# Optimization experiments

Measured on AMD Instinct MI355X. Metric: run time of the kernel, lower is better.

## Reference

```python
import jax, jax.numpy as jnp
import numpy as np

B, C, H, W = 2, 128, 96, 96
HEADS, DHEAD, WIN = 4, 32, 5
INNER = HEADS * DHEAD
PAD = WIN // 2


def setup_inputs() -> dict:
    key = jax.random.key(0)
    k1, k2, k3, k4, k5 = jax.random.split(key, 5)
    s = 1.0 / np.sqrt(C)
    return {
        "x": jax.random.normal(k1, (B, C, H, W), dtype=jnp.float32),
        "wq": jax.random.normal(k2, (INNER, C), dtype=jnp.float32) * s,
        "wk": jax.random.normal(k3, (INNER, C), dtype=jnp.float32) * s,
        "wv": jax.random.normal(k4, (INNER, C), dtype=jnp.float32) * s,
        "wproj": jax.random.normal(k5, (C, INNER), dtype=jnp.float32) * s,
    }


def _windows(t):
    # same neighborhood ordering as F.unfold (row-major over kernel offsets).
    tp = jnp.pad(t, ((0, 0), (0, 0), (0, 0), (PAD, PAD), (PAD, PAD)))
    wins = [tp[:, :, :, di:di + H, dj:dj + W]
            for di in range(WIN) for dj in range(WIN)]
    return jnp.stack(wins, axis=3)


def reference(x, wq, wk, wv, wproj):
    # 1x1 convs == per-pixel linear maps
    q = jnp.einsum('oc,bcxy->boxy', wq, x).reshape(B, HEADS, DHEAD, H, W)
    k = jnp.einsum('oc,bcxy->boxy', wk, x).reshape(B, HEADS, DHEAD, H, W)
    v = jnp.einsum('oc,bcxy->boxy', wv, x).reshape(B, HEADS, DHEAD, H, W)

    k_win = _windows(k)  # (B,h,d,25,H,W)
    v_win = _windows(v)

    scale = 1.0 / np.sqrt(DHEAD)
    attn = jnp.einsum('bhdxy,bhdkxy->bhkxy', q, k_win) * scale
    attn = jax.nn.softmax(attn, axis=2)  # softmax over the 25 window positions
    out = jnp.einsum('bhkxy,bhdkxy->bhdxy', attn, v_win)

    out = out.reshape(B, INNER, H, W)
    return jnp.einsum('co,boxy->bcxy', wproj, out)
```

## Files before the change

### kernel.cpp

```cpp
#include <hip/hip_runtime.h>
#include <hip/hip_bf16.h>
#include <hip/hip_fp16.h>

#define PP 9216
#define OO 384

typedef _Float16 f16x8 __attribute__((ext_vector_type(8)));
typedef _Float16 h2    __attribute__((ext_vector_type(2)));
typedef float    f32x4 __attribute__((ext_vector_type(4)));

#if defined(__has_builtin)
# if __has_builtin(__builtin_amdgcn_fdot2)
#  define HAS_FDOT2 1
# endif
#endif

__device__ __forceinline__ float dot2acc(h2 a, h2 b, float c) {
#ifdef HAS_FDOT2
    return __builtin_amdgcn_fdot2(a, b, c, false);
#else
    return c + (float)a[0] * (float)b[0] + (float)a[1] * (float)b[1];
#endif
}

__global__ __launch_bounds__(256) void prep(
    const float* __restrict__ x, const float* __restrict__ wq,
    const float* __restrict__ wk, const float* __restrict__ wv,
    const float* __restrict__ wp,
    _Float16* __restrict__ xT, _Float16* __restrict__ wqkv,
    _Float16* __restrict__ wproj)
{
    const int t = threadIdx.x;
    if (blockIdx.y == 4) {
        if (blockIdx.z) return;
        int idx = blockIdx.x * 256 + t;
        if (idx < 49152) {
            int o = idx >> 7;
            const float* src = (o < 128) ? wq : ((o < 256) ? wk : wv);
            wqkv[idx] = (_Float16)src[(o & 127) * 128 + (idx & 127)];
        } else if (idx < 65536) {
            int j = idx - 49152;
            wproj[j] = (_Float16)wp[j];
        }
        return;
    }
    __shared__ float sT[32][33];
    const int p0 = blockIdx.x * 32;
    const int c0 = blockIdx.y * 32;
    const int b  = blockIdx.z;
    const int row = t >> 3, col = t & 7;

    const float* xb = x + (size_t)b * 128 * PP;
    float4 v = *(const float4*)(xb + (size_t)(c0 + row) * PP + p0 + col * 4);
    sT[col * 4 + 0][row] = v.x;
    sT[col * 4 + 1][row] = v.y;
    sT[col * 4 + 2][row] = v.z;
    sT[col * 4 + 3][row] = v.w;
    __syncthreads();

    _Float16 h[4];
    #pragma unroll
    for (int j = 0; j < 4; j++) h[j] = (_Float16)sT[row][col * 4 + j];
    *(ushort4*)(xT + (size_t)b * PP * 128 + (size_t)(p0 + row) * 128 + c0 + col * 4) =
        *(ushort4*)h;
}

__global__ __launch_bounds__(256) void qkv_gemm(
    const _Float16* __restrict__ xT, const _Float16* __restrict__ wqkv,
    _Float16* __restrict__ qkv)
{
    const int b = blockIdx.z;
    const int p0 = blockIdx.x * 64;
    const int nbase = blockIdx.y * 192;
    const int t = threadIdx.x;
    const int w = t >> 6, lane = t & 63;
    const int lm = lane & 15, quad = lane >> 4;
    const int ms0 = (w & 1) * 32;
    const int nw = (w >> 1) * 96;

    const _Float16* xb = xT + (size_t)b * PP * 128;
    _Float16* qb = qkv + (size_t)b * PP * OO;

    f16x8 A[2][4];
    #pragma unroll
    for (int ms = 0; ms < 2; ms++)
        #pragma unroll
        for (int kc = 0; kc < 4; kc++)
            A[ms][kc] = *(const f16x8*)(xb + (size_t)(p0 + ms0 + ms * 16 + lm) * 128
                                        + kc * 32 + quad * 8);

    for (int nt = 0; nt < 6; nt++) {
        const int n0 = nbase + nw + nt * 16;
        f16x8 Bf[4];
        #pragma unroll
        for (int kc = 0; kc < 4; kc++)
            Bf[kc] = *(const f16x8*)(wqkv + (size_t)(n0 + lm) * 128 + kc * 32 + quad * 8);
        f32x4 acc[2];
        #pragma unroll
        for (int ms = 0; ms < 2; ms++) {
            acc[ms] = (f32x4){0.f, 0.f, 0.f, 0.f};
            #pragma unroll
            for (int kc = 0; kc < 4; kc++)
                acc[ms] = __builtin_amdgcn_mfma_f32_16x16x32_f16(A[ms][kc], Bf[kc], acc[ms], 0, 0, 0);
        }
        #pragma unroll
        for (int ms = 0; ms < 2; ms++)
            #pragma unroll
            for (int r = 0; r < 4; r++)
                qb[(size_t)(p0 + ms0 + ms * 16 + quad * 4 + r) * OO + n0 + lm] =
                    (_Float16)acc[ms][r];
    }
}

__global__ __launch_bounds__(256) void attn2(
    const _Float16* __restrict__ qkv, _Float16* __restrict__ ao)
{
    __shared__ _Float16 sK[144 * 40];
    __shared__ _Float16 sV[144 * 40];
    __shared__ float sS[64 * 28];

    const int t = threadIdx.x;
    const int x0 = blockIdx.x * 8, y0 = blockIdx.y * 8;
    const int b = blockIdx.z >> 2, h = blockIdx.z & 3;
    const _Float16* base = qkv + (size_t)b * PP * OO;

    for (int u = t; u < 288; u += 256) {
        const int arr = (u >= 144) ? 1 : 0;
        const int pos = u - 144 * arr;
        const int gy = y0 - 2 + pos / 12;
        const int gx = x0 - 2 + pos % 12;
        _Float16* dst = (arr ? sV : sK) + pos * 40;
        if ((unsigned)gy < 96u && (unsigned)gx < 96u) {
            const _Float16* src = base + (size_t)(gy * 96 + gx) * OO + 128 + arr * 128 + h * 32;
            #pragma unroll
            for (int j = 0; j < 4; j++)
                *(uint4*)(dst + j * 8) = *(const uint4*)(src + j * 8);
        } else {
            uint4 z = {0u, 0u, 0u, 0u};
            #pragma unroll
            for (int j = 0; j < 4; j++) *(uint4*)(dst + j * 8) = z;
        }
    }

    const int px = t & 63, w = t >> 6;
    const int ly = px >> 3, lx = px & 7;
    const int gp = (y0 + ly) * 96 + x0 + lx;

    h2 qreg[16];
    {
        const _Float16* qs = base + (size_t)gp * OO + h * 32;
        #pragma unroll
        for (int j = 0; j < 4; j++)
            *(uint4*)(&qreg[j * 4]) = *(const uint4*)(qs + j * 8);
    }
    __syncthreads();

    const float scale = 0.17677669529663689f;
    for (int pos = w; pos < 25; pos += 4) {
        const int hp = (ly + pos / 5) * 12 + lx + pos % 5;
        const _Float16* kr = sK + hp * 40;
        h2 kreg[16];
        #pragma unroll
        for (int j = 0; j < 4; j++)
            *(uint4*)(&kreg[j * 4]) = *(const uint4*)(kr + j * 8);
        float s0 = 0.f, s1 = 0.f;
        #pragma unroll
        for (int j = 0; j < 8; j++) {
            s0 = dot2acc(qreg[2 * j], kreg[2 * j], s0);
            s1 = dot2acc(qreg[2 * j + 1], kreg[2 * j + 1], s1);
        }
        sS[px * 28 + pos] = (s0 + s1) * scale;
    }
    __syncthreads();

    if (t < 64) {
        float* row = sS + t * 28;
        float m = row[0];
        #pragma unroll
        for (int p = 1; p < 25; p++) m = fmaxf(m, row[p]);
        float sum = 0.f;
        float e[25];
        #pragma unroll
        for (int p = 0; p < 25; p++) { e[p] = __expf(row[p] - m); sum += e[p]; }
        const float inv = 1.f / sum;
        #pragma unroll
        for (int p = 0; p < 25; p++) row[p] = e[p] * inv;
    }
    __syncthreads();

    float at[25];
    #pragma unroll
    for (int p = 0; p < 25; p++) at[p] = sS[px * 28 + p];

    float f[8];
    #pragma unroll
    for (int j = 0; j < 8; j++) f[j] = 0.f;
    for (int p = 0; p < 25; p++) {
        const int hp = (ly + p / 5) * 12 + lx + p % 5;
        h2 vreg[4];
        *(uint4*)vreg = *(const uint4*)(sV + hp * 40 + w * 8);
        #pragma unroll
        for (int j = 0; j < 4; j++) {
            f[2 * j]     += at[p] * (float)vreg[j][0];
            f[2 * j + 1] += at[p] * (float)vreg[j][1];
        }
    }
    _Float16 ho[8];
    #pragma unroll
    for (int j = 0; j < 8; j++) ho[j] = (_Float16)f[j];
    *(uint4*)(ao + ((size_t)b * PP + gp) * 128 + h * 32 + w * 8) = *(uint4*)ho;
}

__global__ __launch_bounds__(256) void proj_gemm(
    const _Float16* __restrict__ ao, const _Float16* __restrict__ wproj,
    float* __restrict__ out)
{
    const int b = blockIdx.z;
    const int p0 = blockIdx.x * 64;
    const int t = threadIdx.x;
    const int w = t >> 6, lane = t & 63;
    const int lm = lane & 15, quad = lane >> 4;
    const int ms0 = (w & 1) * 32;
    const int nw = (w >> 1) * 64;

    const _Float16* ab = ao + (size_t)b * PP * 128;
    float* ob = out + (size_t)b * 128 * PP;

    f16x8 A[2][4];
    #pragma unroll
    for (int ms = 0; ms < 2; ms++)
        #pragma unroll
        for (int kc = 0; kc < 4; kc++)
            A[ms][kc] = *(const f16x8*)(ab + (size_t)(p0 + ms0 + ms * 16 + lm) * 128
                                        + kc * 32 + quad * 8);

    for (int nt = 0; nt < 4; nt++) {
        const int n0 = nw + nt * 16;
        f16x8 Bf[4];
        #pragma unroll
        for (int kc = 0; kc < 4; kc++)
            Bf[kc] = *(const f16x8*)(wproj + (size_t)(n0 + lm) * 128 + kc * 32 + quad * 8);
        f32x4 acc[2];
        #pragma unroll
        for (int ms = 0; ms < 2; ms++) {
            acc[ms] = (f32x4){0.f, 0.f, 0.f, 0.f};
            #pragma unroll
            for (int kc = 0; kc < 4; kc++)
                acc[ms] = __builtin_amdgcn_mfma_f32_16x16x32_f16(A[ms][kc], Bf[kc], acc[ms], 0, 0, 0);
        }
        #pragma unroll
        for (int ms = 0; ms < 2; ms++) {
            float4 v = make_float4(acc[ms][0], acc[ms][1], acc[ms][2], acc[ms][3]);
            *(float4*)(ob + (size_t)(n0 + lm) * PP + p0 + ms0 + ms * 16 + quad * 4) = v;
        }
    }
}

extern "C" void kernel_launch(void* const* d_in, const int* in_sizes, int n_in,
                              void* d_out, int out_size, void* d_ws, size_t ws_size,
                              hipStream_t stream)
{
    const float* x  = (const float*)d_in[0];
    const float* wq = (const float*)d_in[1];
    const float* wk = (const float*)d_in[2];
    const float* wv = (const float*)d_in[3];
    const float* wp = (const float*)d_in[4];
    float* out = (float*)d_out;

    _Float16* ws    = (_Float16*)d_ws;
    _Float16* xT    = ws;
    _Float16* wqkv  = xT + 2359296;
    _Float16* wproj = wqkv + 49152;
    _Float16* qkvh  = wproj + 16384;
    _Float16* aoh   = qkvh + 7077888;

    prep<<<dim3(288, 5, 2), 256, 0, stream>>>(x, wq, wk, wv, wp, xT, wqkv, wproj);
    qkv_gemm<<<dim3(144, 2, 2), 256, 0, stream>>>(xT, wqkv, qkvh);
    attn2<<<dim3(12, 12, 8), 256, 0, stream>>>(qkvh, aoh);
    proj_gemm<<<dim3(144, 1, 2), 256, 0, stream>>>(aoh, wproj, out);
}
```

Measured before the change: 107.8 us.

## Fuse attention with output projection and stage QKV epilogue through shared memory

Measured after the change: 110.8 us. 2.8% more time.

```diff
diff --git a/kernel.cpp b/kernel.cpp
--- a/kernel.cpp
+++ b/kernel.cpp
@@ -26,9 +26,7 @@
 __global__ __launch_bounds__(256) void prep(
     const float* __restrict__ x, const float* __restrict__ wq,
     const float* __restrict__ wk, const float* __restrict__ wv,
-    const float* __restrict__ wp,
-    _Float16* __restrict__ xT, _Float16* __restrict__ wqkv,
-    _Float16* __restrict__ wproj)
+    _Float16* __restrict__ xT, _Float16* __restrict__ wqkv)
 {
     const int t = threadIdx.x;
     if (blockIdx.y == 4) {
@@ -38,9 +36,6 @@
             int o = idx >> 7;
             const float* src = (o < 128) ? wq : ((o < 256) ? wk : wv);
             wqkv[idx] = (_Float16)src[(o & 127) * 128 + (idx & 127)];
-        } else if (idx < 65536) {
-            int j = idx - 49152;
-            wproj[j] = (_Float16)wp[j];
         }
         return;
     }
@@ -69,6 +64,8 @@
     const _Float16* __restrict__ xT, const _Float16* __restrict__ wqkv,
     _Float16* __restrict__ qkv)
 {
+    __shared__ _Float16 sEpi[4][32][104];
+
     const int b = blockIdx.z;
     const int p0 = blockIdx.x * 64;
     const int nbase = blockIdx.y * 192;
@@ -107,153 +104,168 @@
         for (int ms = 0; ms < 2; ms++)
             #pragma unroll
             for (int r = 0; r < 4; r++)
-                qb[(size_t)(p0 + ms0 + ms * 16 + quad * 4 + r) * OO + n0 + lm] =
-                    (_Float16)acc[ms][r];
-    }
-}
-
-__global__ __launch_bounds__(256) void attn2(
-    const _Float16* __restrict__ qkv, _Float16* __restrict__ ao)
-{
-    __shared__ _Float16 sK[144 * 40];
-    __shared__ _Float16 sV[144 * 40];
-    __shared__ float sS[64 * 28];
-
-    const int t = threadIdx.x;
-    const int x0 = blockIdx.x * 8, y0 = blockIdx.y * 8;
-    const int b = blockIdx.z >> 2, h = blockIdx.z & 3;
+                sEpi[w][ms * 16 + quad * 4 + r][nt * 16 + lm] = (_Float16)acc[ms][r];
+    }
+
+    #pragma unroll
+    for (int it = 0; it < 6; it++) {
+        int idx = it * 64 + lane;
+        int row = idx / 12;
+        int ch  = idx % 12;
+        uint4 v = *(const uint4*)&sEpi[w][row][ch * 8];
+        *(uint4*)(qb + (size_t)(p0 + ms0 + row) * OO + nbase + nw + ch * 8) = v;
+    }
+}
+
+__global__ __launch_bounds__(256) void attn_proj(
+    const _Float16* __restrict__ qkv, const float* __restrict__ wp,
+    float* __restrict__ out)
+{
+    __shared__ _Float16 sK[96 * 40];
+    __shared__ _Float16 sV[96 * 40];
+    __shared__ float    sS[32 * 29];
+    __shared__ _Float16 sAo[32 * 136];
+
+    const int t  = threadIdx.x;
+    const int x0 = blockIdx.x * 8;
+    const int y0 = blockIdx.y * 4;
+    const int b  = blockIdx.z;
     const _Float16* base = qkv + (size_t)b * PP * OO;
 
-    for (int u = t; u < 288; u += 256) {
-        const int arr = (u >= 144) ? 1 : 0;
-        const int pos = u - 144 * arr;
-        const int gy = y0 - 2 + pos / 12;
-        const int gx = x0 - 2 + pos % 12;
-        _Float16* dst = (arr ? sV : sK) + pos * 40;
-        if ((unsigned)gy < 96u && (unsigned)gx < 96u) {
-            const _Float16* src = base + (size_t)(gy * 96 + gx) * OO + 128 + arr * 128 + h * 32;
+    const int px = t & 31, w8 = t >> 5;
+    const int ly = px >> 3, lx = px & 7;
+    const int gp0 = (y0 + ly) * 96 + x0 + lx;
+    const float scale = 0.17677669529663689f;
+
+    for (int h = 0; h < 4; h++) {
+        if (t < 192) {
+            const int arr = (t >= 96) ? 1 : 0;
+            const int pos = t - 96 * arr;
+            const int gy = y0 - 2 + pos / 12;
+            const int gx = x0 - 2 + pos % 12;
+            _Float16* dst = (arr ? sV : sK) + pos * 40;
+            if ((unsigned)gy < 96u && (unsigned)gx < 96u) {
+                const _Float16* src = base + (size_t)(gy * 96 + gx) * OO + 128 + arr * 128 + h * 32;
+                #pragma unroll
+                for (int j = 0; j < 4; j++)
+                    *(uint4*)(dst + j * 8) = *(const uint4*)(src + j * 8);
+            } else {
+                uint4 z = {0u, 0u, 0u, 0u};
+                #pragma unroll
+                for (int j = 0; j < 4; j++) *(uint4*)(dst + j * 8) = z;
+            }
+        }
+        h2 qreg[16];
+        {
+            const _Float16* qs = base + (size_t)gp0 * OO + h * 32;
             #pragma unroll
             for (int j = 0; j < 4; j++)
-                *(uint4*)(dst + j * 8) = *(const uint4*)(src + j * 8);
-        } else {
-            uint4 z = {0u, 0u, 0u, 0u};
-            #pragma unroll
-            for (int j = 0; j < 4; j++) *(uint4*)(dst + j * 8) = z;
-        }
-    }
-
-    const int px = t & 63, w = t >> 6;
-    const int ly = px >> 3, lx = px & 7;
-    const int gp = (y0 + ly) * 96 + x0 + lx;
-
-    h2 qreg[16];
-    {
-        const _Float16* qs = base + (size_t)gp * OO + h * 32;
-        #pragma unroll
-        for (int j = 0; j < 4; j++)
-            *(uint4*)(&qreg[j * 4]) = *(const uint4*)(qs + j * 8);
-    }
-    __syncthreads();
-
-    const float scale = 0.17677669529663689f;
-    for (int pos = w; pos < 25; pos += 4) {
-        const int hp = (ly + pos / 5) * 12 + lx + pos % 5;
-        const _Float16* kr = sK + hp * 40;
-        h2 kreg[16];
-        #pragma unroll
-        for (int j = 0; j < 4; j++)
-            *(uint4*)(&kreg[j * 4]) = *(const uint4*)(kr + j * 8);
-        float s0 = 0.f, s1 = 0.f;
-        #pragma unroll
-        for (int j = 0; j < 8; j++) {
-            s0 = dot2acc(qreg[2 * j], kreg[2 * j], s0);
-            s1 = dot2acc(qreg[2 * j + 1], kreg[2 * j + 1], s1);
-        }
-        sS[px * 28 + pos] = (s0 + s1) * scale;
-    }
-    __syncthreads();
-
-    if (t < 64) {
-        float* row = sS + t * 28;
-        float m = row[0];
-        #pragma unroll
-        for (int p = 1; p < 25; p++) m = fmaxf(m, row[p]);
-        float sum = 0.f;
-        float e[25];
-        #pragma unroll
-        for (int p = 0; p < 25; p++) { e[p] = __expf(row[p] - m); sum += e[p]; }
-        const float inv = 1.f / sum;
-        #pragma unroll
-        for (int p = 0; p < 25; p++) row[p] = e[p] * inv;
-    }
-    __syncthreads();
-
-    float at[25];
-    #pragma unroll
-    for (int p = 0; p < 25; p++) at[p] = sS[px * 28 + p];
-
-    float f[8];
-    #pragma unroll
-    for (int j = 0; j < 8; j++) f[j] = 0.f;
-    for (int p = 0; p < 25; p++) {
-        const int hp = (ly + p / 5) * 12 + lx + p % 5;
-        h2 vreg[4];
-        *(uint4*)vreg = *(const uint4*)(sV + hp * 40 + w * 8);
-        #pragma unroll
-        for (int j = 0; j < 4; j++) {
-            f[2 * j]     += at[p] * (float)vreg[j][0];
-            f[2 * j + 1] += at[p] * (float)vreg[j][1];
-        }
-    }
-    _Float16 ho[8];
-    #pragma unroll
-    for (int j = 0; j < 8; j++) ho[j] = (_Float16)f[j];
-    *(uint4*)(ao + ((size_t)b * PP + gp) * 128 + h * 32 + w * 8) = *(uint4*)ho;
-}
-
-__global__ __launch_bounds__(256) void proj_gemm(
-    const _Float16* __restrict__ ao, const _Float16* __restrict__ wproj,
-    float* __restrict__ out)
-{
-    const int b = blockIdx.z;
-    const int p0 = blockIdx.x * 64;
-    const int t = threadIdx.x;
-    const int w = t >> 6, lane = t & 63;
+                *(uint4*)(&qreg[j * 4]) = *(const uint4*)(qs + j * 8);
+        }
+        __syncthreads();
+
+        for (int pos = w8; pos < 25; pos += 8) {
+            const int hp = (ly + pos / 5) * 12 + lx + pos % 5;
+            const _Float16* kr = sK + hp * 40;
+            h2 kreg[16];
+            #pragma unroll
+            for (int j = 0; j < 4; j++)
+                *(uint4*)(&kreg[j * 4]) = *(const uint4*)(kr + j * 8);
+            float s0 = 0.f, s1 = 0.f;
+            #pragma unroll
+            for (int j = 0; j < 8; j++) {
+                s0 = dot2acc(qreg[2 * j], kreg[2 * j], s0);
+                s1 = dot2acc(qreg[2 * j + 1], kreg[2 * j + 1], s1);
+            }
+            sS[px * 29 + pos] = (s0 + s1) * scale;
+        }
+        __syncthreads();
+
+        if (t < 32) {
+            float* row = sS + t * 29;
+            float m = row[0];
+            #pragma unroll
+            for (int p = 1; p < 25; p++) m = fmaxf(m, row[p]);
+            float sum = 0.f;
+            float e[25];
+            #pragma unroll
+            for (int p = 0; p < 25; p++) { e[p] = __expf(row[p] - m); sum += e[p]; }
+            const float inv = 1.f / sum;
+            #pragma unroll
+            for (int p = 0; p < 25; p++) row[p] = e[p] * inv;
+        }
+        __syncthreads();
+
+        float at[25];
+        #pragma unroll
+        for (int p = 0; p < 25; p++) at[p] = sS[px * 29 + p];
+
+        float f[4] = {0.f, 0.f, 0.f, 0.f};
+        for (int p = 0; p < 25; p++) {
+            const int hp = (ly + p / 5) * 12 + lx + p % 5;
+            h2 vreg[2];
+            *(uint2*)vreg = *(const uint2*)(sV + hp * 40 + w8 * 4);
+            #pragma unroll
+            for (int j = 0; j < 2; j++) {
+                f[2 * j]     += at[p] * (float)vreg[j][0];
+                f[2 * j + 1] += at[p] * (float)vreg[j][1];
+            }
+        }
+        _Float16 ho[4];
+        #pragma unroll
+        for (int j = 0; j < 4; j++) ho[j] = (_Float16)f[j];
+        *(ushort4*)(sAo + px * 136 + h * 32 + w8 * 4) = *(ushort4*)ho;
+        __syncthreads();
+    }
+
+    const int lane = t & 63, w4 = t >> 6;
     const int lm = lane & 15, quad = lane >> 4;
-    const int ms0 = (w & 1) * 32;
-    const int nw = (w >> 1) * 64;
-
-    const _Float16* ab = ao + (size_t)b * PP * 128;
+
+    f16x8 Aw[2][4];
+    #pragma unroll
+    for (int mt = 0; mt < 2; mt++)
+        #pragma unroll
+        for (int kc = 0; kc < 4; kc++) {
+            const float* ws_ = wp + (size_t)(w4 * 32 + mt * 16 + lm) * 128 + kc * 32 + quad * 8;
+            float4 a0 = *(const float4*)ws_;
+            float4 a1 = *(const float4*)(ws_ + 4);
+            Aw[mt][kc] = (f16x8){(_Float16)a0.x, (_Float16)a0.y, (_Float16)a0.z, (_Float16)a0.w,
+                                 (_Float16)a1.x, (_Float16)a1.y, (_Float16)a1.z, (_Float16)a1.w};
+        }
+
+    f32x4 acc[2][2];
+    #pragma unroll
+    for (int mt = 0; mt < 2; mt++)
+        #pragma unroll
+        for (int nt = 0; nt < 2; nt++)
+            acc[mt][nt] = (f32x4){0.f, 0.f, 0.f, 0.f};
+
+    #pragma unroll
+    for (int nt = 0; nt < 2; nt++) {
+        f16x8 Bf[4];
+        #pragma unroll
+        for (int kc = 0; kc < 4; kc++)
+            Bf[kc] = *(const f16x8*)(sAo + (nt * 16 + lm) * 136 + kc * 32 + quad * 8);
+        #pragma unroll
+        for (int mt = 0; mt < 2; mt++)
+            #pragma unroll
+            for (int kc = 0; kc < 4; kc++)
+                acc[mt][nt] = __builtin_amdgcn_mfma_f32_16x16x32_f16(Aw[mt][kc], Bf[kc], acc[mt][nt], 0, 0, 0);
+    }
+
     float* ob = out + (size_t)b * 128 * PP;
-
-    f16x8 A[2][4];
-    #pragma unroll
-    for (int ms = 0; ms < 2; ms++)
-        #pragma unroll
-        for (int kc = 0; kc < 4; kc++)
-            A[ms][kc] = *(const f16x8*)(ab + (size_t)(p0 + ms0 + ms * 16 + lm) * 128
-                                        + kc * 32 + quad * 8);
-
-    for (int nt = 0; nt < 4; nt++) {
-        const int n0 = nw + nt * 16;
-        f16x8 Bf[4];
-        #pragma unroll
-        for (int kc = 0; kc < 4; kc++)
-            Bf[kc] = *(const f16x8*)(wproj + (size_t)(n0 + lm) * 128 + kc * 32 + quad * 8);
-        f32x4 acc[2];
-        #pragma unroll
-        for (int ms = 0; ms < 2; ms++) {
-            acc[ms] = (f32x4){0.f, 0.f, 0.f, 0.f};
-            #pragma unroll
-            for (int kc = 0; kc < 4; kc++)
-                acc[ms] = __builtin_amdgcn_mfma_f32_16x16x32_f16(A[ms][kc], Bf[kc], acc[ms], 0, 0, 0);
-        }
-        #pragma unroll
-        for (int ms = 0; ms < 2; ms++) {
-            float4 v = make_float4(acc[ms][0], acc[ms][1], acc[ms][2], acc[ms][3]);
-            *(float4*)(ob + (size_t)(n0 + lm) * PP + p0 + ms0 + ms * 16 + quad * 4) = v;
-        }
-    }
+    #pragma unroll
+    for (int mt = 0; mt < 2; mt++)
+        #pragma unroll
+        for (int nt = 0; nt < 2; nt++) {
+            const int pxl = nt * 16 + lm;
+            const int gpl = (y0 + (pxl >> 3)) * 96 + x0 + (pxl & 7);
+            #pragma unroll
+            for (int r = 0; r < 4; r++) {
+                const int c = w4 * 32 + mt * 16 + quad * 4 + r;
+                ob[(size_t)c * PP + gpl] = acc[mt][nt][r];
+            }
+        }
 }
 
 extern "C" void kernel_launch(void* const* d_in, const int* in_sizes, int n_in,
@@ -270,12 +282,9 @@
     _Float16* ws    = (_Float16*)d_ws;
     _Float16* xT    = ws;
     _Float16* wqkv  = xT + 2359296;
-    _Float16* wproj = wqkv + 49152;
-    _Float16* qkvh  = wproj + 16384;
-    _Float16* aoh   = qkvh + 7077888;
-
-    prep<<<dim3(288, 5, 2), 256, 0, stream>>>(x, wq, wk, wv, wp, xT, wqkv, wproj);
+    _Float16* qkvh  = wqkv + 49152;
+
+    prep<<<dim3(288, 5, 2), 256, 0, stream>>>(x, wq, wk, wv, xT, wqkv);
     qkv_gemm<<<dim3(144, 2, 2), 256, 0, stream>>>(xT, wqkv, qkvh);
-    attn2<<<dim3(12, 12, 8), 256, 0, stream>>>(qkvh, aoh);
-    proj_gemm<<<dim3(144, 1, 2), 256, 0, stream>>>(aoh, wproj, out);
-}
+    attn_proj<<<dim3(12, 24, 2), 256, 0, stream>>>(qkvh, wp, out);
+}
```
